# Kernel optimization log

Hardware: AMD Instinct MI355X
Metric: run time of the kernel (lower is better)

The kernel has to match this reference:

```python
import jax, jax.numpy as jnp
import numpy as np

# db2 DWT filter taps and contrast-masking kernel (buffers from __init__)
_LO = np.array([0.48296291314469, 0.836516303737469, 0.224143868041857, -0.129409522550921], dtype=np.float32)
_HI = np.array([-0.129409522550921, -0.224143868041857, 0.836516303737469, -0.48296291314469], dtype=np.float32)
_CM = np.array([[1/30, 1/30, 1/30], [1/30, 1/15, 1/30], [1/30, 1/30, 1/30]], dtype=np.float32).reshape(1, 1, 3, 3)
_RF = [[0.017382, 0.017382, 0.005891], [0.031985, 0.031985, 0.014299],
       [0.043373, 0.043373, 0.024397], [0.045673, 0.045673, 0.031313]]
_EPS = 1e-30
_GAIN = 100.0  # adm_enhn_gain_limit, NEG=False
_COS1SQ = float(np.cos(np.pi / 180.0) ** 2)


def _pad(x, l, r, t, b):  # vmaf_pad: reflect padding on H,W of NCHW
    return jnp.pad(x, ((0, 0), (0, 0), (t, b), (l, r)), mode='reflect')


def _conv(x, w, stride):
    return jax.lax.conv_general_dilated(x, jnp.asarray(w), stride, 'VALID',
                                        dimension_numbers=('NCHW', 'OIHW', 'NCHW'))


def _dwt2(X):
    """Separable db2 DWT: returns (approx, horizontal, vertical, diagonal)."""
    pb = 1 if X.shape[-2] % 2 == 0 else 2
    Xp = _pad(X, 0, 0, 1, pb)
    lo_v = _conv(Xp, _LO.reshape(1, 1, 4, 1), (2, 1))
    hi_v = _conv(Xp, _HI.reshape(1, 1, 4, 1), (2, 1))
    pr = 1 if lo_v.shape[-1] % 2 == 0 else 2
    hor = lambda Y, f: _conv(_pad(Y, 1, pr, 0, 0), f.reshape(1, 1, 1, 4), (1, 2))
    return hor(lo_v, _LO), hor(hi_v, _LO), hor(lo_v, _HI), hor(hi_v, _HI)  # a, h, v, d


def _decouple(Oh, Ov, Od, Th, Tv, Td):
    Kh = jnp.clip(Th / (Oh + _EPS), 0.0, 1.0)
    Kv = jnp.clip(Tv / (Ov + _EPS), 0.0, 1.0)
    Kd = jnp.clip(Td / (Od + _EPS), 0.0, 1.0)
    Rh, Rv, Rd = Kh * Oh, Kv * Ov, Kd * Od
    ot = Oh * Th + Ov * Tv
    flag = (ot >= 0.0) & (ot * ot >= _COS1SQ * (Oh * Oh + Ov * Ov) * (Th * Th + Tv * Tv))

    def gain(R, T):
        R = jnp.where(flag & (R > 0.0), jnp.minimum(R * _GAIN, T), R)
        return jnp.where(flag & (R < 0.0), jnp.maximum(R * _GAIN, T), R)

    Rh, Rv, Rd = gain(Rh, Th), gain(Rv, Tv), gain(Rd, Td)
    return Rh, Rv, Rd, Th - Rh, Tv - Rv, Td - Rd


def _border(w, h):
    left = int(np.floor(w * 0.1 - 0.5))
    top = int(np.floor(h * 0.1 - 0.5))
    right, bottom = w - left, h - top
    ih, iv = jnp.arange(w), jnp.arange(h)
    mask = ((ih < left) | (ih >= right))[None, :] | ((iv < top) | (iv >= bottom))[:, None]
    return mask, left, top, right, bottom


def _norm3(x):  # Minkowski pooling, p=3 over spatial dims -> [b,1]
    return jnp.power(jnp.sum(jnp.abs(x) ** 3, axis=(-1, -2)), 1.0 / 3.0)


def _csf_den(Oh, Ov, Od, scale):
    h, w = Oh.shape[-2], Oh.shape[-1]
    mask, left, top, right, bottom = _border(w, h)
    rf = _RF[scale]
    den = sum(_norm3(jnp.where(mask, 0.0, r * O)) for r, O in zip(rf, (Oh, Ov, Od)))
    return den + 3.0 * (((bottom - top) * (right - left)) / 32.0) ** (1.0 / 3.0)


def _cm_num(Rh, Rv, Rd, Ah, Av, Ad, scale):
    rf = _RF[scale]
    h, w = Rh.shape[-2], Rh.shape[-1]
    mask, left, top, right, bottom = _border(w, h)
    num = 0.0
    for r, R, A in zip(rf, (Rh, Rv, Rd), (Ah, Av, Ad)):
        thr = _conv(jnp.abs(_pad(r * A, 1, 1, 1, 1)), _CM, (1, 1))  # contrast-masking threshold
        thr = jnp.where(mask, 0.0, thr)
        Rm = jnp.where(mask, 0.0, R)
        num = num + _norm3(jnp.maximum(jnp.abs(r * Rm) - thr, 0.0))
    return num + 3.0 * (((bottom - top) * (right - left)) / 32.0) ** (1.0 / 3.0)


def _num_den(X_ref, X_dst):
    Oa, Ta = X_ref, X_dst
    nums, dens = [], []
    for scale in range(4):
        Oa, Oh, Ov, Od = _dwt2(Oa)
        Ta, Th, Tv, Td = _dwt2(Ta)
        Rh, Rv, Rd, Ah, Av, Ad = _decouple(Oh, Ov, Od, Th, Tv, Td)
        dens.append(_csf_den(Oh, Ov, Od, scale))
        nums.append(_cm_num(Rh, Rv, Rd, Ah, Av, Ad, scale))
    return jnp.concatenate(nums, -1), jnp.concatenate(dens, -1)  # each [b, 4]


def setup_inputs() -> dict:
    key = jax.random.key(0)
    k1, k2 = jax.random.split(key)
    X_ref = jax.random.uniform(k1, (4, 1, 1080, 1920), dtype=jnp.float32) * 255.0
    # distorted = reference + noise, a realistic VQA setting
    X_dst = jnp.clip(X_ref + 5.0 * jax.random.normal(k2, X_ref.shape, dtype=jnp.float32), 0.0, 255.0)
    return {"X_ref": X_ref, "X_dst": X_dst}


def reference(X_ref, X_dst):
    H, W = X_ref.shape[-2], X_ref.shape[-1]
    num, den = _num_den(X_ref, X_dst)
    num_sum = num.sum(-1, keepdims=True)
    den_sum = den.sum(-1, keepdims=True)
    lim = 1e-10 * (W * H) / (1920 * 1080)
    num_sum = jnp.where(num_sum < lim, 0.0, num_sum)
    den_sum = jnp.where(den_sum < lim, 0.0, den_sum)
    safe_den = jnp.where(den_sum == 0.0, 1.0, den_sum)
    return jnp.where(den_sum == 0.0, 1.0, num_sum / safe_den)  # [b, 1]
```

## Files before the change

### kernel.cpp

```cpp
#include <hip/hip_runtime.h>
#include <math.h>

#define BATCH 4
#define S0 (540 * 960)
#define REPL 32

#define FBX 32
#define FBY 16
#define NTHR 512
#define HTW 34
#define HTH 18
#define HTP 36
#define SRW 70
#define VP  72

__device__ __forceinline__ int reflect_idx(int i, int n) {
    if (i < 0) i = -i;
    if (i >= n) i = 2 * n - 2 - i;
    return i;
}

__device__ __forceinline__ void decouple6(float oh, float ov, float od,
                                          float th, float tv, float td,
                                          float& Rh, float& Rv, float& Rd,
                                          float& Ah, float& Av, float& Ad)
{
    const float EPS = 1e-30f;
    const float COS1SQ = 0.9996954135095479f;

    float kh = th / (oh + EPS); kh = fminf(fmaxf(kh, 0.f), 1.f);
    float kv = tv / (ov + EPS); kv = fminf(fmaxf(kv, 0.f), 1.f);
    float kd = td / (od + EPS); kd = fminf(fmaxf(kd, 0.f), 1.f);
    float rh = kh * oh, rv = kv * ov, rd = kd * od;

    float ot = oh * th + ov * tv;
    bool flag = (ot >= 0.f) &&
                (ot * ot >= COS1SQ * (oh * oh + ov * ov) * (th * th + tv * tv));
    if (flag) {
        if (rh > 0.f) rh = fminf(rh * 100.f, th);
        if (rh < 0.f) rh = fmaxf(rh * 100.f, th);
        if (rv > 0.f) rv = fminf(rv * 100.f, tv);
        if (rv < 0.f) rv = fmaxf(rv * 100.f, tv);
        if (rd > 0.f) rd = fminf(rd * 100.f, td);
        if (rd < 0.f) rd = fmaxf(rd * 100.f, td);
    }
    Rh = rh; Rv = rv; Rd = rd;
    Ah = th - rh; Av = tv - rv; Ad = td - rd;
}

__global__ __launch_bounds__(NTHR) void
fused_kernel(const float* __restrict__ srcR, const float* __restrict__ srcD,
             long srcBatchStride, int H, int W, int H2, int W2,
             float* __restrict__ outAR, float* __restrict__ outAD,
             int left, int top, int right, int bottom,
             float rfh, float rfv, float rfd,
             float* __restrict__ acc, int scale)
{
    const float LO0 =  0.48296291314469f,  LO1 =  0.836516303737469f,
                LO2 =  0.224143868041857f, LO3 = -0.129409522550921f;
    const float HI0 = -0.129409522550921f, HI1 = -0.224143868041857f,
                HI2 =  0.836516303737469f, HI3 = -0.48296291314469f;

    __shared__ float sVloR[HTH][VP], sVhiR[HTH][VP];
    __shared__ float sVloD[HTH][VP], sVhiD[HTH][VP];
    __shared__ float sh[HTH][HTP], sv[HTH][HTP], sd[HTH][HTP];
    __shared__ float srh[HTH][HTP], srv[HTH][HTP], srd[HTH][HTP];
    __shared__ float smem[8][6];

    int b  = blockIdx.z;
    int X0 = blockIdx.x * FBX;
    int Y0 = blockIdx.y * FBY;
    int tid = threadIdx.y * FBX + threadIdx.x;

    const float* pR = srcR + (long)b * srcBatchStride;
    const float* pD = srcD + (long)b * srcBatchStride;

    for (int i = tid; i < SRW * HTH; i += NTHR) {
        int c = i % SRW, ly = i / SRW;
        int gc = reflect_idx(2 * X0 - 3 + c, W);
        int rb = 2 * Y0 + 2 * ly - 3;
        long q0 = (long)reflect_idx(rb + 0, H) * W + gc;
        long q1 = (long)reflect_idx(rb + 1, H) * W + gc;
        long q2 = (long)reflect_idx(rb + 2, H) * W + gc;
        long q3 = (long)reflect_idx(rb + 3, H) * W + gc;
        float r0 = pR[q0], r1 = pR[q1], r2 = pR[q2], r3 = pR[q3];
        sVloR[ly][c] = LO0 * r0 + LO1 * r1 + LO2 * r2 + LO3 * r3;
        sVhiR[ly][c] = HI0 * r0 + HI1 * r1 + HI2 * r2 + HI3 * r3;
        float d0 = pD[q0], d1 = pD[q1], d2 = pD[q2], d3 = pD[q3];
        sVloD[ly][c] = LO0 * d0 + LO1 * d1 + LO2 * d2 + LO3 * d3;
        sVhiD[ly][c] = HI0 * d0 + HI1 * d1 + HI2 * d2 + HI3 * d3;
    }
    __syncthreads();

    float denh = 0.f, denv = 0.f, dend = 0.f;
    float numh = 0.f, numv = 0.f, numd = 0.f;
    long base2 = (long)b * S0;

    for (int i = tid; i < HTW * HTH; i += NTHR) {
        int lx = i % HTW, ly = i / HTW;
        int cc = 2 * lx;

        float l0 = sVloR[ly][cc], l1 = sVloR[ly][cc + 1],
              l2 = sVloR[ly][cc + 2], l3 = sVloR[ly][cc + 3];
        float h0 = sVhiR[ly][cc], h1 = sVhiR[ly][cc + 1],
              h2 = sVhiR[ly][cc + 2], h3 = sVhiR[ly][cc + 3];
        float aR = LO0 * l0 + LO1 * l1 + LO2 * l2 + LO3 * l3;
        float ov = HI0 * l0 + HI1 * l1 + HI2 * l2 + HI3 * l3;
        float oh = LO0 * h0 + LO1 * h1 + LO2 * h2 + LO3 * h3;
        float od = HI0 * h0 + HI1 * h1 + HI2 * h2 + HI3 * h3;

        l0 = sVloD[ly][cc]; l1 = sVloD[ly][cc + 1];
        l2 = sVloD[ly][cc + 2]; l3 = sVloD[ly][cc + 3];
        h0 = sVhiD[ly][cc]; h1 = sVhiD[ly][cc + 1];
        h2 = sVhiD[ly][cc + 2]; h3 = sVhiD[ly][cc + 3];
        float aD = LO0 * l0 + LO1 * l1 + LO2 * l2 + LO3 * l3;
        float tv = HI0 * l0 + HI1 * l1 + HI2 * l2 + HI3 * l3;
        float th = LO0 * h0 + LO1 * h1 + LO2 * h2 + LO3 * h3;
        float td = HI0 * h0 + HI1 * h1 + HI2 * h2 + HI3 * h3;

        float rh, rv, rd, ah, av, ad;
        decouple6(oh, ov, od, th, tv, td, rh, rv, rd, ah, av, ad);
        sh[ly][lx]  = fabsf(rfh * ah);
        sv[ly][lx]  = fabsf(rfv * av);
        sd[ly][lx]  = fabsf(rfd * ad);
        srh[ly][lx] = rh;
        srv[ly][lx] = rv;
        srd[ly][lx] = rd;

        int bx = X0 - 1 + lx, by = Y0 - 1 + ly;
        bool center = (lx >= 1) && (lx <= FBX) && (ly >= 1) && (ly <= FBY);
        if (center && bx < W2 && by < H2) {
            long o = base2 + (long)by * W2 + bx;
            outAR[o] = aR;
            outAD[o] = aD;
            if (bx >= left && bx < right && by >= top && by < bottom) {
                float t;
                t = fabsf(rfh * oh); denh += t * t * t;
                t = fabsf(rfv * ov); denv += t * t * t;
                t = fabsf(rfd * od); dend += t * t * t;
            }
        }
    }
    __syncthreads();

    {
        int bx = X0 + threadIdx.x, by = Y0 + threadIdx.y;
        if (bx >= left && bx < right && by >= top && by < bottom) {
            int lx = threadIdx.x + 1, ly = threadIdx.y + 1;
            const float w0 = 1.f / 30.f, wc = 1.f / 15.f;
            float thrh = wc * sh[ly][lx] + w0 * (sh[ly-1][lx-1] + sh[ly-1][lx] + sh[ly-1][lx+1] +
                                                 sh[ly][lx-1]   + sh[ly][lx+1] +
                                                 sh[ly+1][lx-1] + sh[ly+1][lx] + sh[ly+1][lx+1]);
            float thrv = wc * sv[ly][lx] + w0 * (sv[ly-1][lx-1] + sv[ly-1][lx] + sv[ly-1][lx+1] +
                                                 sv[ly][lx-1]   + sv[ly][lx+1] +
                                                 sv[ly+1][lx-1] + sv[ly+1][lx] + sv[ly+1][lx+1]);
            float thrd = wc * sd[ly][lx] + w0 * (sd[ly-1][lx-1] + sd[ly-1][lx] + sd[ly-1][lx+1] +
                                                 sd[ly][lx-1]   + sd[ly][lx+1] +
                                                 sd[ly+1][lx-1] + sd[ly+1][lx] + sd[ly+1][lx+1]);
            float t;
            t = fmaxf(fabsf(rfh * srh[ly][lx]) - thrh, 0.f); numh = t * t * t;
            t = fmaxf(fabsf(rfv * srv[ly][lx]) - thrv, 0.f); numv = t * t * t;
            t = fmaxf(fabsf(rfd * srd[ly][lx]) - thrd, 0.f); numd = t * t * t;
        }
    }

    float vals[6] = {denh, denv, dend, numh, numv, numd};
    #pragma unroll
    for (int i = 0; i < 6; ++i) {
        float v = vals[i];
        #pragma unroll
        for (int off = 32; off > 0; off >>= 1) v += __shfl_down(v, off, 64);
        vals[i] = v;
    }
    __syncthreads();
    if ((tid & 63) == 0) {
        #pragma unroll
        for (int i = 0; i < 6; ++i) smem[tid >> 6][i] = vals[i];
    }
    __syncthreads();
    if (tid < 6) {
        float s = 0.f;
        #pragma unroll
        for (int w = 0; w < 8; ++w) s += smem[w][tid];
        int repl = (blockIdx.y * gridDim.x + blockIdx.x) % REPL;
        atomicAdd(&acc[(((long)repl * BATCH + b) * 4 + scale) * 6 + tid], s);
    }
}

__global__ void zero_kernel(float* __restrict__ acc)
{
    int i = blockIdx.x * blockDim.x + threadIdx.x;
    if (i < REPL * BATCH * 4 * 6) acc[i] = 0.f;
}

__global__ void final_kernel(const float* __restrict__ acc, float* __restrict__ out,
                             float c0, float c1, float c2, float c3)
{
    __shared__ float tot[BATCH][4][6];
    int t = threadIdx.x;
    if (t < BATCH * 4 * 6) {
        int k = t % 6, s = (t / 6) % 4, b = t / 24;
        float v = 0.f;
        for (int r = 0; r < REPL; ++r)
            v += acc[(((long)r * BATCH + b) * 4 + s) * 6 + k];
        tot[b][s][k] = v;
    }
    __syncthreads();
    if (t < BATCH) {
        float cs[4] = {c0, c1, c2, c3};
        float num = 0.f, den = 0.f;
        for (int s = 0; s < 4; ++s) {
            den += cbrtf(tot[t][s][0]) + cbrtf(tot[t][s][1]) + cbrtf(tot[t][s][2]) + cs[s];
            num += cbrtf(tot[t][s][3]) + cbrtf(tot[t][s][4]) + cbrtf(tot[t][s][5]) + cs[s];
        }
        const float lim = 1e-10f;
        if (num < lim) num = 0.f;
        if (den < lim) den = 0.f;
        out[t] = (den == 0.f) ? 1.f : num / den;
    }
}

extern "C" void kernel_launch(void* const* d_in, const int* in_sizes, int n_in,
                              void* d_out, int out_size, void* d_ws, size_t ws_size,
                              hipStream_t stream)
{
    const float* Xref = (const float*)d_in[0];
    const float* Xdst = (const float*)d_in[1];
    float* out = (float*)d_out;
    float* ws  = (float*)d_ws;

    float* aRefA = ws + (long)0 * BATCH * S0;
    float* aRefB = ws + (long)1 * BATCH * S0;
    float* aDstA = ws + (long)2 * BATCH * S0;
    float* aDstB = ws + (long)3 * BATCH * S0;
    float* acc   = ws + (long)4 * BATCH * S0;

    zero_kernel<<<dim3((REPL * BATCH * 24 + 255) / 256), dim3(256), 0, stream>>>(acc);

    static const float RF[4][3] = {
        {0.017382f, 0.017382f, 0.005891f},
        {0.031985f, 0.031985f, 0.014299f},
        {0.043373f, 0.043373f, 0.024397f},
        {0.045673f, 0.045673f, 0.031313f}};

    int H = 1080, W = 1920;
    long srcStride = (long)H * W;
    const float* sR = Xref;
    const float* sD = Xdst;
    float* pingR[2] = {aRefA, aRefB};
    float* pingD[2] = {aDstA, aDstB};
    float cs[4];

    for (int s = 0; s < 4; ++s) {
        int H2 = (H + 1) / 2, W2 = (W + 1) / 2;
        float* oR = pingR[s & 1];
        float* oD = pingD[s & 1];

        int left   = (int)floor((double)W2 * 0.1 - 0.5);
        int top    = (int)floor((double)H2 * 0.1 - 0.5);
        int right  = W2 - left;
        int bottom = H2 - top;

        dim3 blk(FBX, FBY), grd((W2 + FBX - 1) / FBX, (H2 + FBY - 1) / FBY, BATCH);
        fused_kernel<<<grd, blk, 0, stream>>>(sR, sD, srcStride, H, W, H2, W2,
                                              oR, oD, left, top, right, bottom,
                                              RF[s][0], RF[s][1], RF[s][2], acc, s);

        cs[s] = 3.0f * cbrtf((float)((long)(bottom - top) * (right - left)) / 32.0f);

        sR = oR; sD = oD; srcStride = S0;
        H = H2; W = W2;
    }

    final_kernel<<<dim3(1), dim3(128), 0, stream>>>(acc, out, cs[0], cs[1], cs[2], cs[3]);
}
```

Measured before the change: 73.15 us.

## Add interior fast path, two-row vertical DWT per thread, packed float2 smem

Tiles away from the image border now skip the reflect-index math in the load phase. Each thread now computes two vertical DWT output rows from six input rows, which reuses the two rows the outputs share and halves the number of loop iterations. The six per-pixel shared arrays are packed into three float2 arrays with an odd pitch, so the 3x3 masking stencil needs fewer LDS instructions and has fewer bank conflicts. Index arithmetic moves from 64-bit to 32-bit, which is safe at this problem size but removes the guard against overflow on larger inputs.

```diff
diff --git a/kernel.cpp b/kernel.cpp
--- a/kernel.cpp
+++ b/kernel.cpp
@@ -10,7 +10,7 @@
 #define NTHR 512
 #define HTW 34
 #define HTH 18
-#define HTP 36
+#define HTP 35
 #define SRW 70
 #define VP  72
 
@@ -63,8 +63,9 @@
 
     __shared__ float sVloR[HTH][VP], sVhiR[HTH][VP];
     __shared__ float sVloD[HTH][VP], sVhiD[HTH][VP];
-    __shared__ float sh[HTH][HTP], sv[HTH][HTP], sd[HTH][HTP];
-    __shared__ float srh[HTH][HTP], srv[HTH][HTP], srd[HTH][HTP];
+    __shared__ float2 sA[HTH][HTP];
+    __shared__ float2 sB[HTH][HTP];
+    __shared__ float2 sC[HTH][HTP];
     __shared__ float smem[8][6];
 
     int b  = blockIdx.z;
@@ -75,26 +76,59 @@
     const float* pR = srcR + (long)b * srcBatchStride;
     const float* pD = srcD + (long)b * srcBatchStride;
 
-    for (int i = tid; i < SRW * HTH; i += NTHR) {
-        int c = i % SRW, ly = i / SRW;
-        int gc = reflect_idx(2 * X0 - 3 + c, W);
-        int rb = 2 * Y0 + 2 * ly - 3;
-        long q0 = (long)reflect_idx(rb + 0, H) * W + gc;
-        long q1 = (long)reflect_idx(rb + 1, H) * W + gc;
-        long q2 = (long)reflect_idx(rb + 2, H) * W + gc;
-        long q3 = (long)reflect_idx(rb + 3, H) * W + gc;
-        float r0 = pR[q0], r1 = pR[q1], r2 = pR[q2], r3 = pR[q3];
-        sVloR[ly][c] = LO0 * r0 + LO1 * r1 + LO2 * r2 + LO3 * r3;
-        sVhiR[ly][c] = HI0 * r0 + HI1 * r1 + HI2 * r2 + HI3 * r3;
-        float d0 = pD[q0], d1 = pD[q1], d2 = pD[q2], d3 = pD[q3];
-        sVloD[ly][c] = LO0 * d0 + LO1 * d1 + LO2 * d2 + LO3 * d3;
-        sVhiD[ly][c] = HI0 * d0 + HI1 * d1 + HI2 * d2 + HI3 * d3;
+    bool interior = (X0 >= 2) && (2 * X0 + SRW - 4 < W) &&
+                    (Y0 >= 2) && (2 * Y0 + 4 * (HTH / 2 - 1) + 2 < H);
+    if (interior) {
+        for (int i = tid; i < SRW * (HTH / 2); i += NTHR) {
+            int c = i % SRW, lp = i / SRW;
+            int ly = 2 * lp;
+            int gc = 2 * X0 - 3 + c;
+            int rb = 2 * Y0 + 4 * lp - 3;
+            int q = rb * W + gc;
+            float r0 = pR[q], r1 = pR[q + W], r2 = pR[q + 2 * W],
+                  r3 = pR[q + 3 * W], r4 = pR[q + 4 * W], r5 = pR[q + 5 * W];
+            sVloR[ly][c]     = LO0 * r0 + LO1 * r1 + LO2 * r2 + LO3 * r3;
+            sVhiR[ly][c]     = HI0 * r0 + HI1 * r1 + HI2 * r2 + HI3 * r3;
+            sVloR[ly + 1][c] = LO0 * r2 + LO1 * r3 + LO2 * r4 + LO3 * r5;
+            sVhiR[ly + 1][c] = HI0 * r2 + HI1 * r3 + HI2 * r4 + HI3 * r5;
+            float d0 = pD[q], d1 = pD[q + W], d2 = pD[q + 2 * W],
+                  d3 = pD[q + 3 * W], d4 = pD[q + 4 * W], d5 = pD[q + 5 * W];
+            sVloD[ly][c]     = LO0 * d0 + LO1 * d1 + LO2 * d2 + LO3 * d3;
+            sVhiD[ly][c]     = HI0 * d0 + HI1 * d1 + HI2 * d2 + HI3 * d3;
+            sVloD[ly + 1][c] = LO0 * d2 + LO1 * d3 + LO2 * d4 + LO3 * d5;
+            sVhiD[ly + 1][c] = HI0 * d2 + HI1 * d3 + HI2 * d4 + HI3 * d5;
+        }
+    } else {
+        for (int i = tid; i < SRW * (HTH / 2); i += NTHR) {
+            int c = i % SRW, lp = i / SRW;
+            int ly = 2 * lp;
+            int gc = reflect_idx(2 * X0 - 3 + c, W);
+            int rb = 2 * Y0 + 4 * lp - 3;
+            int q0 = reflect_idx(rb + 0, H) * W + gc;
+            int q1 = reflect_idx(rb + 1, H) * W + gc;
+            int q2 = reflect_idx(rb + 2, H) * W + gc;
+            int q3 = reflect_idx(rb + 3, H) * W + gc;
+            int q4 = reflect_idx(rb + 4, H) * W + gc;
+            int q5 = reflect_idx(rb + 5, H) * W + gc;
+            float r0 = pR[q0], r1 = pR[q1], r2 = pR[q2],
+                  r3 = pR[q3], r4 = pR[q4], r5 = pR[q5];
+            sVloR[ly][c]     = LO0 * r0 + LO1 * r1 + LO2 * r2 + LO3 * r3;
+            sVhiR[ly][c]     = HI0 * r0 + HI1 * r1 + HI2 * r2 + HI3 * r3;
+            sVloR[ly + 1][c] = LO0 * r2 + LO1 * r3 + LO2 * r4 + LO3 * r5;
+            sVhiR[ly + 1][c] = HI0 * r2 + HI1 * r3 + HI2 * r4 + HI3 * r5;
+            float d0 = pD[q0], d1 = pD[q1], d2 = pD[q2],
+                  d3 = pD[q3], d4 = pD[q4], d5 = pD[q5];
+            sVloD[ly][c]     = LO0 * d0 + LO1 * d1 + LO2 * d2 + LO3 * d3;
+            sVhiD[ly][c]     = HI0 * d0 + HI1 * d1 + HI2 * d2 + HI3 * d3;
+            sVloD[ly + 1][c] = LO0 * d2 + LO1 * d3 + LO2 * d4 + LO3 * d5;
+            sVhiD[ly + 1][c] = HI0 * d2 + HI1 * d3 + HI2 * d4 + HI3 * d5;
+        }
     }
     __syncthreads();
 
     float denh = 0.f, denv = 0.f, dend = 0.f;
     float numh = 0.f, numv = 0.f, numd = 0.f;
-    long base2 = (long)b * S0;
+    int base2 = b * S0;
 
     for (int i = tid; i < HTW * HTH; i += NTHR) {
         int lx = i % HTW, ly = i / HTW;
@@ -120,17 +154,14 @@
 
         float rh, rv, rd, ah, av, ad;
         decouple6(oh, ov, od, th, tv, td, rh, rv, rd, ah, av, ad);
-        sh[ly][lx]  = fabsf(rfh * ah);
-        sv[ly][lx]  = fabsf(rfv * av);
-        sd[ly][lx]  = fabsf(rfd * ad);
-        srh[ly][lx] = rh;
-        srv[ly][lx] = rv;
-        srd[ly][lx] = rd;
+        sA[ly][lx] = make_float2(fabsf(rfh * ah), fabsf(rfv * av));
+        sB[ly][lx] = make_float2(fabsf(rfd * ad), rh);
+        sC[ly][lx] = make_float2(rv, rd);
 
         int bx = X0 - 1 + lx, by = Y0 - 1 + ly;
         bool center = (lx >= 1) && (lx <= FBX) && (ly >= 1) && (ly <= FBY);
         if (center && bx < W2 && by < H2) {
-            long o = base2 + (long)by * W2 + bx;
+            int o = base2 + by * W2 + bx;
             outAR[o] = aR;
             outAD[o] = aD;
             if (bx >= left && bx < right && by >= top && by < bottom) {
@@ -148,19 +179,23 @@
         if (bx >= left && bx < right && by >= top && by < bottom) {
             int lx = threadIdx.x + 1, ly = threadIdx.y + 1;
             const float w0 = 1.f / 30.f, wc = 1.f / 15.f;
-            float thrh = wc * sh[ly][lx] + w0 * (sh[ly-1][lx-1] + sh[ly-1][lx] + sh[ly-1][lx+1] +
-                                                 sh[ly][lx-1]   + sh[ly][lx+1] +
-                                                 sh[ly+1][lx-1] + sh[ly+1][lx] + sh[ly+1][lx+1]);
-            float thrv = wc * sv[ly][lx] + w0 * (sv[ly-1][lx-1] + sv[ly-1][lx] + sv[ly-1][lx+1] +
-                                                 sv[ly][lx-1]   + sv[ly][lx+1] +
-                                                 sv[ly+1][lx-1] + sv[ly+1][lx] + sv[ly+1][lx+1]);
-            float thrd = wc * sd[ly][lx] + w0 * (sd[ly-1][lx-1] + sd[ly-1][lx] + sd[ly-1][lx+1] +
-                                                 sd[ly][lx-1]   + sd[ly][lx+1] +
-                                                 sd[ly+1][lx-1] + sd[ly+1][lx] + sd[ly+1][lx+1]);
+            float2 a00 = sA[ly-1][lx-1], a01 = sA[ly-1][lx], a02 = sA[ly-1][lx+1];
+            float2 a10 = sA[ly  ][lx-1], a11 = sA[ly  ][lx], a12 = sA[ly  ][lx+1];
+            float2 a20 = sA[ly+1][lx-1], a21 = sA[ly+1][lx], a22 = sA[ly+1][lx+1];
+            float thrh = wc * a11.x + w0 * (a00.x + a01.x + a02.x + a10.x + a12.x +
+                                            a20.x + a21.x + a22.x);
+            float thrv = wc * a11.y + w0 * (a00.y + a01.y + a02.y + a10.y + a12.y +
+                                            a20.y + a21.y + a22.y);
+            float2 b00 = sB[ly-1][lx-1], b01 = sB[ly-1][lx], b02 = sB[ly-1][lx+1];
+            float2 b10 = sB[ly  ][lx-1], b11 = sB[ly  ][lx], b12 = sB[ly  ][lx+1];
+            float2 b20 = sB[ly+1][lx-1], b21 = sB[ly+1][lx], b22 = sB[ly+1][lx+1];
+            float thrd = wc * b11.x + w0 * (b00.x + b01.x + b02.x + b10.x + b12.x +
+                                            b20.x + b21.x + b22.x);
+            float2 cc_ = sC[ly][lx];
             float t;
-            t = fmaxf(fabsf(rfh * srh[ly][lx]) - thrh, 0.f); numh = t * t * t;
-            t = fmaxf(fabsf(rfv * srv[ly][lx]) - thrv, 0.f); numv = t * t * t;
-            t = fmaxf(fabsf(rfd * srd[ly][lx]) - thrd, 0.f); numd = t * t * t;
+            t = fmaxf(fabsf(rfh * b11.y) - thrh, 0.f); numh = t * t * t;
+            t = fmaxf(fabsf(rfv * cc_.x) - thrv, 0.f); numv = t * t * t;
+            t = fmaxf(fabsf(rfd * cc_.y) - thrd, 0.f); numd = t * t * t;
         }
     }
 
```

Result: faster. 68.42 us (-6.5%).
